# Performance work log

Hardware: AMD Instinct MI355X
Metric: run time of the kernel (lower is better)

Reference implementation:

```python
import math
import jax, jax.numpy as jnp
import numpy as np

TEMPERATURE = 1.0  # matches init kwarg

S, B, T, D = 16, 4, 1024, 2048


def setup_inputs() -> dict:
    key = jax.random.key(0)
    k1, k2 = jax.random.split(key)
    layer_query = jax.random.normal(k1, (D,), dtype=jnp.float32)
    source_bank = jax.random.normal(k2, (S, B, T, D), dtype=jnp.float32)
    return {"layer_query": layer_query, "source_bank": source_bank, "num_sources": S}


def reference(layer_query, source_bank, num_sources):
    # RMSNorm over last dim of the key bank (torch F.rms_norm with eps=None
    # uses the dtype's machine epsilon)
    eps = jnp.finfo(source_bank.dtype).eps
    ms = jnp.mean(jnp.square(source_bank), axis=-1, keepdims=True)  # [s,b,t,1]
    keys = source_bank * jax.lax.rsqrt(ms + eps)
    d = source_bank.shape[-1]
    scale = 1.0 / (math.sqrt(d) * TEMPERATURE)
    query = layer_query.astype(source_bank.dtype)
    scores = jnp.einsum('d,sbtd->sbt', query, keys) * scale  # [s,b,t]
    weights = jax.nn.softmax(scores, axis=0)                 # softmax over sources
    mixed = jnp.einsum('sbt,sbtd->btd', weights, source_bank)
    return mixed
```

## Files before the change

kernel.cpp:

```cpp
#include <hip/hip_runtime.h>


#define NSRC 16
#define NB   4
#define NT   1024
#define ND   2048

typedef __fp16 half2_t __attribute__((ext_vector_type(2)));

__global__ __launch_bounds__(1024, 8)
void dar_fused_kernel(const float* __restrict__ q,
                      const float* __restrict__ bank,
                      float* __restrict__ out) {
    __shared__ half2_t lds[NSRC * (ND / 2)];
    __shared__ float s_scores[NSRC];

    const int bt   = blockIdx.x;
    const int tid  = threadIdx.x;
    const int wave = tid >> 6;
    const int lane = tid & 63;

    const float4* src = reinterpret_cast<const float4*>(
        bank + ((size_t)wave * NB * NT + bt) * ND);
    const float4* q4  = reinterpret_cast<const float4*>(q);
    half2_t* ldsrow   = lds + wave * (ND / 2);

    float p2 = 0.0f, pq = 0.0f;
    #pragma unroll
    for (int i = 0; i < 8; ++i) {
        const int d4 = i * 64 + lane;
        const float4 v  = src[d4];
        const float4 qv = q4[d4];
        p2 += v.x * v.x + v.y * v.y + v.z * v.z + v.w * v.w;
        pq += qv.x * v.x + qv.y * v.y + qv.z * v.z + qv.w * v.w;
        ldsrow[d4 * 2 + 0] = __builtin_amdgcn_cvt_pkrtz(v.x, v.y);
        ldsrow[d4 * 2 + 1] = __builtin_amdgcn_cvt_pkrtz(v.z, v.w);
    }

    #pragma unroll
    for (int m = 32; m >= 1; m >>= 1) {
        p2 += __shfl_xor(p2, m, 64);
        pq += __shfl_xor(pq, m, 64);
    }
    if (lane == 0) {
        const float ms  = p2 * (1.0f / ND) + 1.1920928955078125e-07f;
        s_scores[wave]  = pq * rsqrtf(ms) * 0.022097086912079608f;
    }
    __syncthreads();

    float w[NSRC];
    float mx = -1e30f;
    #pragma unroll
    for (int s = 0; s < NSRC; ++s) { w[s] = s_scores[s]; mx = fmaxf(mx, w[s]); }
    float sum = 0.0f;
    #pragma unroll
    for (int s = 0; s < NSRC; ++s) { w[s] = __expf(w[s] - mx); sum += w[s]; }
    const float inv = 1.0f / sum;

    float ax = 0.0f, ay = 0.0f;
    #pragma unroll
    for (int s = 0; s < NSRC; ++s) {
        const half2_t h = lds[s * (ND / 2) + tid];
        ax += w[s] * (float)h.x;
        ay += w[s] * (float)h.y;
    }
    float2 r;
    r.x = ax * inv;
    r.y = ay * inv;
    reinterpret_cast<float2*>(out + (size_t)bt * ND)[tid] = r;
}

extern "C" void kernel_launch(void* const* d_in, const int* in_sizes, int n_in,
                              void* d_out, int out_size, void* d_ws, size_t ws_size,
                              hipStream_t stream) {
    const float* q    = (const float*)d_in[0];
    const float* bank = (const float*)d_in[1];
    float* out        = (float*)d_out;

    dim3 grid(NB * NT);
    dim3 block(1024);
    dar_fused_kernel<<<grid, block, 0, stream>>>(q, bank, out);
}
```

Before: 111.4 us.

## Make kernel persistent with register prefetch and double-buffered LDS across tiles

Replaces the one-block-per-(b,t) launch with 256 persistent blocks that each process 16 consecutive (b,t) tiles. The next tile's bank rows are prefetched into registers while the current tile is mixed, and the fp16 LDS staging and score buffers are double-buffered so one barrier per tile suffices. The query is held in registers across tiles. The intent is to hide memory latency and cut block launch overhead, but the 128 KB LDS footprint limits residency to one block per CU, which reduces memory-level parallelism.

```diff
diff --git a/kernel.cpp b/kernel.cpp
--- a/kernel.cpp
+++ b/kernel.cpp
@@ -1,73 +1,105 @@
 #include <hip/hip_runtime.h>
+#include <stdint.h>
 
 
-#define NSRC 16
-#define NB   4
-#define NT   1024
-#define ND   2048
+#define NSRC  16
+#define NB    4
+#define NT    1024
+#define ND    2048
+#define TILES 16
+#define NBLK  256
 
 typedef __fp16 half2_t __attribute__((ext_vector_type(2)));
 
-__global__ __launch_bounds__(1024, 8)
-void dar_fused_kernel(const float* __restrict__ q,
-                      const float* __restrict__ bank,
-                      float* __restrict__ out) {
-    __shared__ half2_t lds[NSRC * (ND / 2)];
-    __shared__ float s_scores[NSRC];
+__global__ __launch_bounds__(1024, 4)
+void dar_persist_kernel(const float* __restrict__ q,
+                        const float* __restrict__ bank,
+                        float* __restrict__ out) {
+    __shared__ __align__(16) uint32_t buf[2][NSRC][ND / 2];
+    __shared__ float s_sc[2][NSRC];
 
-    const int bt   = blockIdx.x;
     const int tid  = threadIdx.x;
     const int wave = tid >> 6;
     const int lane = tid & 63;
+    const int bt0  = blockIdx.x * TILES;
 
-    const float4* src = reinterpret_cast<const float4*>(
-        bank + ((size_t)wave * NB * NT + bt) * ND);
-    const float4* q4  = reinterpret_cast<const float4*>(q);
-    half2_t* ldsrow   = lds + wave * (ND / 2);
+    const float4* q4 = reinterpret_cast<const float4*>(q);
+    float4 qr[8];
+    #pragma unroll
+    for (int i = 0; i < 8; ++i) qr[i] = q4[i * 64 + lane];
 
-    float p2 = 0.0f, pq = 0.0f;
+    const float4* srcbase = reinterpret_cast<const float4*>(bank)
+                          + ((size_t)wave * (NB * NT) + bt0) * (ND / 4);
+
+    float4 rA[8], rB[8];
     #pragma unroll
-    for (int i = 0; i < 8; ++i) {
-        const int d4 = i * 64 + lane;
-        const float4 v  = src[d4];
-        const float4 qv = q4[d4];
-        p2 += v.x * v.x + v.y * v.y + v.z * v.z + v.w * v.w;
-        pq += qv.x * v.x + qv.y * v.y + qv.z * v.z + qv.w * v.w;
-        ldsrow[d4 * 2 + 0] = __builtin_amdgcn_cvt_pkrtz(v.x, v.y);
-        ldsrow[d4 * 2 + 1] = __builtin_amdgcn_cvt_pkrtz(v.z, v.w);
+    for (int i = 0; i < 8; ++i) rA[i] = srcbase[i * 64 + lane];
+
+    auto body = [&](int t, float4 (&cur)[8], float4 (&nxt)[8]) {
+        const int c  = t & 1;
+        const int bt = bt0 + t;
+
+        float p2 = 0.0f, pq = 0.0f;
+        #pragma unroll
+        for (int i = 0; i < 8; ++i) {
+            const float4 v = cur[i], qv = qr[i];
+            p2 += v.x * v.x + v.y * v.y + v.z * v.z + v.w * v.w;
+            pq += qv.x * v.x + qv.y * v.y + qv.z * v.z + qv.w * v.w;
+        }
+        #pragma unroll
+        for (int m = 32; m >= 1; m >>= 1) {
+            p2 += __shfl_xor(p2, m, 64);
+            pq += __shfl_xor(pq, m, 64);
+        }
+        if (lane == 0) {
+            const float ms = p2 * (1.0f / ND) + 1.1920928955078125e-07f;
+            s_sc[c][wave]  = pq * rsqrtf(ms) * 0.022097086912079608f;
+        }
+
+        #pragma unroll
+        for (int i = 0; i < 8; ++i) {
+            const float4 v = cur[i];
+            const half2_t lo = __builtin_amdgcn_cvt_pkrtz(v.x, v.y);
+            const half2_t hi = __builtin_amdgcn_cvt_pkrtz(v.z, v.w);
+            uint2 u;
+            u.x = __builtin_bit_cast(uint32_t, lo);
+            u.y = __builtin_bit_cast(uint32_t, hi);
+            reinterpret_cast<uint2*>(&buf[c][wave][0])[i * 64 + lane] = u;
+        }
+
+        __syncthreads();
+
+        if (t + 1 < TILES) {
+            const float4* s2 = srcbase + (size_t)(t + 1) * (ND / 4);
+            #pragma unroll
+            for (int i = 0; i < 8; ++i) nxt[i] = s2[i * 64 + lane];
+        }
+
+        float w[NSRC], mx = -1e30f;
+        #pragma unroll
+        for (int s = 0; s < NSRC; ++s) { w[s] = s_sc[c][s]; mx = fmaxf(mx, w[s]); }
+        float sum = 0.0f;
+        #pragma unroll
+        for (int s = 0; s < NSRC; ++s) { w[s] = __expf(w[s] - mx); sum += w[s]; }
+        const float inv = 1.0f / sum;
+
+        float ax = 0.0f, ay = 0.0f;
+        #pragma unroll
+        for (int s = 0; s < NSRC; ++s) {
+            const half2_t h = __builtin_bit_cast(half2_t, buf[c][s][tid]);
+            ax += w[s] * (float)h.x;
+            ay += w[s] * (float)h.y;
+        }
+        float2 r;
+        r.x = ax * inv;
+        r.y = ay * inv;
+        reinterpret_cast<float2*>(out + (size_t)bt * ND)[tid] = r;
+    };
+
+    for (int tt = 0; tt < TILES; tt += 2) {
+        body(tt,     rA, rB);
+        body(tt + 1, rB, rA);
     }
-
-    #pragma unroll
-    for (int m = 32; m >= 1; m >>= 1) {
-        p2 += __shfl_xor(p2, m, 64);
-        pq += __shfl_xor(pq, m, 64);
-    }
-    if (lane == 0) {
-        const float ms  = p2 * (1.0f / ND) + 1.1920928955078125e-07f;
-        s_scores[wave]  = pq * rsqrtf(ms) * 0.022097086912079608f;
-    }
-    __syncthreads();
-
-    float w[NSRC];
-    float mx = -1e30f;
-    #pragma unroll
-    for (int s = 0; s < NSRC; ++s) { w[s] = s_scores[s]; mx = fmaxf(mx, w[s]); }
-    float sum = 0.0f;
-    #pragma unroll
-    for (int s = 0; s < NSRC; ++s) { w[s] = __expf(w[s] - mx); sum += w[s]; }
-    const float inv = 1.0f / sum;
-
-    float ax = 0.0f, ay = 0.0f;
-    #pragma unroll
-    for (int s = 0; s < NSRC; ++s) {
-        const half2_t h = lds[s * (ND / 2) + tid];
-        ax += w[s] * (float)h.x;
-        ay += w[s] * (float)h.y;
-    }
-    float2 r;
-    r.x = ax * inv;
-    r.y = ay * inv;
-    reinterpret_cast<float2*>(out + (size_t)bt * ND)[tid] = r;
 }
 
 extern "C" void kernel_launch(void* const* d_in, const int* in_sizes, int n_in,
@@ -77,7 +109,7 @@
     const float* bank = (const float*)d_in[1];
     float* out        = (float*)d_out;
 
-    dim3 grid(NB * NT);
+    dim3 grid(NBLK);
     dim3 block(1024);
-    dar_fused_kernel<<<grid, block, 0, stream>>>(q, bank, out);
+    dar_persist_kernel<<<grid, block, 0, stream>>>(q, bank, out);
 }
```

New measurement: 122.4 us. +9.8%, slower.
